# Optimization experiments

Measured on AMD Instinct MI355X. Metric: run time of the kernel, lower is better.

## Reference

```python
import jax, jax.numpy as jnp
import numpy as np

INPUT_DIM = 100
LATENT_DIM = 128
HIDDEN_DIM = 64
BATCH = 16384


def setup_inputs() -> dict:
    key = jax.random.key(0)
    ku, k1, kb1, k2, kb2 = jax.random.split(key, 5)
    u = jax.random.normal(ku, (BATCH, INPUT_DIM), dtype=jnp.float32)
    # PyTorch Linear init: U(-1/sqrt(fan_in), 1/sqrt(fan_in))
    s1 = 1.0 / np.sqrt(INPUT_DIM)
    s2 = 1.0 / np.sqrt(HIDDEN_DIM)
    W1 = jax.random.uniform(k1, (LATENT_DIM, HIDDEN_DIM, INPUT_DIM), jnp.float32, -s1, s1)
    b1 = jax.random.uniform(kb1, (LATENT_DIM, HIDDEN_DIM), jnp.float32, -s1, s1)
    W2 = jax.random.uniform(k2, (LATENT_DIM, HIDDEN_DIM), jnp.float32, -s2, s2)  # out_features=1 squeezed
    b2 = jax.random.uniform(kb2, (LATENT_DIM,), jnp.float32, -s2, s2)
    return {"u": u, "W1": W1, "b1": b1, "W2": W2, "b2": b2}


def reference(u, W1, b1, W2, b2):
    # All latent_dim branches batched as one grouped GEMM.
    # h: [batch, latent, hidden]
    h = jnp.tanh(jnp.einsum('bi,khi->bkh', u, W1) + b1[None, :, :])
    # out: [batch, latent]  (second Linear has output dim 1, squeezed)
    out = jnp.einsum('bkh,kh->bk', h, W2) + b2[None, :]
    return out
```

## Files before the change

kernel.cpp:

```cpp
#include <hip/hip_runtime.h>

#define BATCH 16384
#define LATENT 128
#define HIDDEN 64
#define INDIM 100
#define KPAD 128
#define TANH_SCALE 2.885390081777927f

typedef short shortx8 __attribute__((ext_vector_type(8)));
typedef float floatx4 __attribute__((ext_vector_type(4)));

__device__ __forceinline__ short f2bf(float f) {
    union { float f; unsigned u; } v; v.f = f;
    unsigned r = v.u + 0x7FFF + ((v.u >> 16) & 1);
    return (short)(r >> 16);
}

#if __has_builtin(__builtin_amdgcn_exp2f)
#define EXP2F(x) __builtin_amdgcn_exp2f(x)
#else
#define EXP2F(x) __exp2f(x)
#endif
#if __has_builtin(__builtin_amdgcn_rcpf)
#define RCPF(x) __builtin_amdgcn_rcpf(x)
#else
#define RCPF(x) (1.0f / (x))
#endif

#define N_U_CHUNKS (BATCH * KPAD / 8)
#define N_W_CHUNKS (LATENT * HIDDEN * KPAD / 8)

__global__ __launch_bounds__(256) void prep_all(const float* __restrict__ u,
                                                const float* __restrict__ W1,
                                                const float* __restrict__ b1,
                                                const float* __restrict__ W2,
                                                const float* __restrict__ b2,
                                                shortx8* __restrict__ uf,
                                                shortx8* __restrict__ wf,
                                                float* __restrict__ b2eff) {
    int c = blockIdx.x * 256 + threadIdx.x;
    if (c < N_U_CHUNKS) {
        int lane = c & 63;
        int kt = (c >> 6) & 3;
        int g = c >> 8;
        int row = g * 16 + (lane & 15);
        int kbase = kt * 32 + ((lane >> 4) << 3);
        shortx8 v;
        if (kbase + 7 < INDIM) {
            const float4* p = (const float4*)(u + row * INDIM + kbase);
            float4 f0 = p[0], f1 = p[1];
            v[0] = f2bf(f0.x); v[1] = f2bf(f0.y); v[2] = f2bf(f0.z); v[3] = f2bf(f0.w);
            v[4] = f2bf(f1.x); v[5] = f2bf(f1.y); v[6] = f2bf(f1.z); v[7] = f2bf(f1.w);
        } else {
#pragma unroll
            for (int j = 0; j < 8; j++) {
                int k = kbase + j;
                float f = (k < INDIM) ? u[row * INDIM + k] : (k == INDIM ? 1.0f : 0.0f);
                v[j] = f2bf(f);
            }
        }
        uf[c] = v;
    } else if (c < N_U_CHUNKS + N_W_CHUNKS) {
        int c2 = c - N_U_CHUNKS;
        int lane = c2 & 63;
        int kt = (c2 >> 6) & 3;
        int nt = (c2 >> 8) & 3;
        int lat = c2 >> 10;
        int h = nt * 16 + (lane & 15);
        int hw = lat * HIDDEN + h;
        int kbase = kt * 32 + ((lane >> 4) << 3);
        shortx8 v;
        if (kbase + 7 < INDIM) {
            const float4* p = (const float4*)(W1 + hw * INDIM + kbase);
            float4 f0 = p[0], f1 = p[1];
            v[0] = f2bf(f0.x * TANH_SCALE); v[1] = f2bf(f0.y * TANH_SCALE);
            v[2] = f2bf(f0.z * TANH_SCALE); v[3] = f2bf(f0.w * TANH_SCALE);
            v[4] = f2bf(f1.x * TANH_SCALE); v[5] = f2bf(f1.y * TANH_SCALE);
            v[6] = f2bf(f1.z * TANH_SCALE); v[7] = f2bf(f1.w * TANH_SCALE);
        } else {
#pragma unroll
            for (int j = 0; j < 8; j++) {
                int k = kbase + j;
                float f = (k < INDIM) ? W1[hw * INDIM + k] * TANH_SCALE
                                      : (k == INDIM ? b1[hw] * TANH_SCALE : 0.0f);
                v[j] = f2bf(f);
            }
        }
        wf[c2] = v;
    } else {
        int lat = c - (N_U_CHUNKS + N_W_CHUNKS);
        if (lat < LATENT) {
            float s = b2[lat];
            const float* wp = W2 + lat * HIDDEN;
#pragma unroll 8
            for (int h = 0; h < HIDDEN; h++) s += wp[h];
            b2eff[lat] = s;
        }
    }
}

__global__ __launch_bounds__(256, 4) void branch_mlp(const shortx8* __restrict__ uf,
                                                     const shortx8* __restrict__ wf,
                                                     const float* __restrict__ W2,
                                                     const float* __restrict__ b2eff,
                                                     float* __restrict__ out) {
    int tid = threadIdx.x;
    int lane = tid & 63;
    int w = tid >> 6;
    int bx = blockIdx.x;
    int lat = bx >> 5;
    int G0 = (bx & 31) * 32 + w * 8;
    int q = lane >> 4;

    shortx8 afr[4][4];
    const shortx8* wb = wf + (size_t)lat * 16 * 64 + lane;
#pragma unroll
    for (int nt = 0; nt < 4; nt++)
#pragma unroll
        for (int kt = 0; kt < 4; kt++)
            afr[nt][kt] = wb[(nt * 4 + kt) * 64];

    float4 w2v[4];
#pragma unroll
    for (int nt = 0; nt < 4; nt++) {
        float4 t = *(const float4*)(W2 + lat * HIDDEN + nt * 16 + q * 4);
        w2v[nt] = make_float4(-2.0f * t.x, -2.0f * t.y, -2.0f * t.z, -2.0f * t.w);
    }
    float b2v = b2eff[lat];

    const shortx8* ua = uf + (size_t)G0 * 4 * 64 + lane;
    float* outp = out + (size_t)G0 * 16 * LATENT + lat;

#pragma unroll
    for (int g = 0; g < 8; g++) {
        shortx8 ub[4];
#pragma unroll
        for (int kt = 0; kt < 4; kt++)
            ub[kt] = ua[(g * 4 + kt) * 64];

        floatx4 acc[4] = {};
#pragma unroll
        for (int kt = 0; kt < 4; kt++)
#pragma unroll
            for (int nt = 0; nt < 4; nt++)
                acc[nt] = __builtin_amdgcn_mfma_f32_16x16x32_bf16(afr[nt][kt], ub[kt], acc[nt], 0, 0, 0);

        float s = 0.0f;
#pragma unroll
        for (int nt = 0; nt < 4; nt++)
#pragma unroll
            for (int r = 0; r < 4; r++) {
                float e = EXP2F(acc[nt][r]);
                float rr = RCPF(e + 1.0f);
                s = fmaf((&w2v[nt].x)[r], rr, s);
            }
        s += __shfl_xor(s, 16, 64);
        s += __shfl_xor(s, 32, 64);
        if (lane < 16)
            outp[(g * 16 + lane) * LATENT] = s + b2v;
    }
}

__global__ __launch_bounds__(256) void fallback_kernel(const float* __restrict__ u, const float* __restrict__ W1,
                                                       const float* __restrict__ b1, const float* __restrict__ W2,
                                                       const float* __restrict__ b2, float* __restrict__ out) {
    int idx = blockIdx.x * 256 + threadIdx.x;
    if (idx >= BATCH * LATENT) return;
    int b = idx >> 7;
    int lat = idx & 127;
    const float* ub = u + b * INDIM;
    float s = 0.0f;
    for (int h = 0; h < HIDDEN; h++) {
        const float* wp = W1 + (lat * HIDDEN + h) * INDIM;
        float dd = b1[lat * HIDDEN + h];
        for (int k = 0; k < INDIM; k++) dd += ub[k] * wp[k];
        s += tanhf(dd) * W2[lat * HIDDEN + h];
    }
    out[idx] = s + b2[lat];
}

extern "C" void kernel_launch(void* const* d_in, const int* in_sizes, int n_in,
                              void* d_out, int out_size, void* d_ws, size_t ws_size,
                              hipStream_t stream) {
    const float* u  = (const float*)d_in[0];
    const float* W1 = (const float*)d_in[1];
    const float* b1 = (const float*)d_in[2];
    const float* W2 = (const float*)d_in[3];
    const float* b2 = (const float*)d_in[4];
    float* out = (float*)d_out;

    const size_t UF_BYTES = (size_t)BATCH * KPAD * 2;
    const size_t WF_BYTES = (size_t)LATENT * HIDDEN * KPAD * 2;
    const size_t B2_BYTES = LATENT * sizeof(float);

    if (ws_size < UF_BYTES + WF_BYTES + B2_BYTES) {
        fallback_kernel<<<(BATCH * LATENT + 255) / 256, 256, 0, stream>>>(u, W1, b1, W2, b2, out);
        return;
    }

    shortx8* uf = (shortx8*)d_ws;
    shortx8* wf = (shortx8*)((char*)d_ws + UF_BYTES);
    float* b2eff = (float*)((char*)d_ws + UF_BYTES + WF_BYTES);

    prep_all<<<(N_U_CHUNKS + N_W_CHUNKS) / 256 + 1, 256, 0, stream>>>(u, W1, b1, W2, b2, uf, wf, b2eff);
    branch_mlp<<<4096, 256, 0, stream>>>(uf, wf, W2, b2eff, out);
}
```

Measured before the change: 112.8 us.

## Stage prep conversion through LDS for coalesced loads and batch output shuffles

The prep kernel now processes 16-row tiles per block. It reads the fp32 rows with coalesced float2 loads, converts them to bf16 into a padded LDS tile, then writes the MFMA fragment layout from LDS. The old version had each thread gather strided float4 pairs from scattered rows. In the main kernel, the cross-lane reductions and output stores for all 8 groups are deferred until after the compute loop, so the shuffles are batched and the loop can overlap better. The cost is one LDS buffer and a barrier in prep, plus 8 extra live registers in the main kernel.

```diff
diff --git a/kernel.cpp b/kernel.cpp
--- a/kernel.cpp
+++ b/kernel.cpp
@@ -10,10 +10,9 @@
 typedef short shortx8 __attribute__((ext_vector_type(8)));
 typedef float floatx4 __attribute__((ext_vector_type(4)));
 
-__device__ __forceinline__ short f2bf(float f) {
+__device__ __forceinline__ unsigned bfbits(float f) {
     union { float f; unsigned u; } v; v.f = f;
-    unsigned r = v.u + 0x7FFF + ((v.u >> 16) & 1);
-    return (short)(r >> 16);
+    return (v.u + 0x7FFF + ((v.u >> 16) & 1)) >> 16;
 }
 
 #if __has_builtin(__builtin_amdgcn_exp2f)
@@ -27,8 +26,8 @@
 #define RCPF(x) (1.0f / (x))
 #endif
 
-#define N_U_CHUNKS (BATCH * KPAD / 8)
-#define N_W_CHUNKS (LATENT * HIDDEN * KPAD / 8)
+#define N_U_BLK (BATCH / 16)
+#define N_W_BLK (LATENT * HIDDEN / 16)
 
 __global__ __launch_bounds__(256) void prep_all(const float* __restrict__ u,
                                                 const float* __restrict__ W1,
@@ -38,64 +37,52 @@
                                                 shortx8* __restrict__ uf,
                                                 shortx8* __restrict__ wf,
                                                 float* __restrict__ b2eff) {
-    int c = blockIdx.x * 256 + threadIdx.x;
-    if (c < N_U_CHUNKS) {
-        int lane = c & 63;
-        int kt = (c >> 6) & 3;
-        int g = c >> 8;
-        int row = g * 16 + (lane & 15);
-        int kbase = kt * 32 + ((lane >> 4) << 3);
-        shortx8 v;
-        if (kbase + 7 < INDIM) {
-            const float4* p = (const float4*)(u + row * INDIM + kbase);
-            float4 f0 = p[0], f1 = p[1];
-            v[0] = f2bf(f0.x); v[1] = f2bf(f0.y); v[2] = f2bf(f0.z); v[3] = f2bf(f0.w);
-            v[4] = f2bf(f1.x); v[5] = f2bf(f1.y); v[6] = f2bf(f1.z); v[7] = f2bf(f1.w);
-        } else {
-#pragma unroll
-            for (int j = 0; j < 8; j++) {
-                int k = kbase + j;
-                float f = (k < INDIM) ? u[row * INDIM + k] : (k == INDIM ? 1.0f : 0.0f);
-                v[j] = f2bf(f);
-            }
-        }
-        uf[c] = v;
-    } else if (c < N_U_CHUNKS + N_W_CHUNKS) {
-        int c2 = c - N_U_CHUNKS;
-        int lane = c2 & 63;
-        int kt = (c2 >> 6) & 3;
-        int nt = (c2 >> 8) & 3;
-        int lat = c2 >> 10;
-        int h = nt * 16 + (lane & 15);
-        int hw = lat * HIDDEN + h;
-        int kbase = kt * 32 + ((lane >> 4) << 3);
-        shortx8 v;
-        if (kbase + 7 < INDIM) {
-            const float4* p = (const float4*)(W1 + hw * INDIM + kbase);
-            float4 f0 = p[0], f1 = p[1];
-            v[0] = f2bf(f0.x * TANH_SCALE); v[1] = f2bf(f0.y * TANH_SCALE);
-            v[2] = f2bf(f0.z * TANH_SCALE); v[3] = f2bf(f0.w * TANH_SCALE);
-            v[4] = f2bf(f1.x * TANH_SCALE); v[5] = f2bf(f1.y * TANH_SCALE);
-            v[6] = f2bf(f1.z * TANH_SCALE); v[7] = f2bf(f1.w * TANH_SCALE);
-        } else {
-#pragma unroll
-            for (int j = 0; j < 8; j++) {
-                int k = kbase + j;
-                float f = (k < INDIM) ? W1[hw * INDIM + k] * TANH_SCALE
-                                      : (k == INDIM ? b1[hw] * TANH_SCALE : 0.0f);
-                v[j] = f2bf(f);
-            }
-        }
-        wf[c2] = v;
-    } else {
-        int lat = c - (N_U_CHUNKS + N_W_CHUNKS);
-        if (lat < LATENT) {
-            float s = b2[lat];
-            const float* wp = W2 + lat * HIDDEN;
+    int bx = blockIdx.x;
+    int tid = threadIdx.x;
+
+    if (bx >= N_U_BLK + N_W_BLK) {
+        if (tid < LATENT) {
+            float s = b2[tid];
+            const float* wp = W2 + tid * HIDDEN;
 #pragma unroll 8
             for (int h = 0; h < HIDDEN; h++) s += wp[h];
-            b2eff[lat] = s;
+            b2eff[tid] = s;
         }
+        return;
+    }
+
+    bool isW = (bx >= N_U_BLK);
+    int tileIdx = isW ? (bx - N_U_BLK) : bx;
+    int r0 = tileIdx * 16;
+    const float* src = isW ? W1 : u;
+    float scale = isW ? TANH_SCALE : 1.0f;
+
+    __shared__ short lds[16 * 136];
+
+#pragma unroll
+    for (int it = 0; it < 4; it++) {
+        int p = it * 256 + tid;
+        int rl = p >> 6;
+        int kp = (p & 63) * 2;
+        float f0 = 0.0f, f1 = 0.0f;
+        if (kp < INDIM) {
+            const float2 t = *(const float2*)(src + (r0 + rl) * INDIM + kp);
+            f0 = t.x * scale; f1 = t.y * scale;
+        } else if (kp == INDIM) {
+            f0 = isW ? b1[r0 + rl] * TANH_SCALE : 1.0f;
+        }
+        *(unsigned*)(&lds[rl * 136 + kp]) = bfbits(f0) | (bfbits(f1) << 16);
+    }
+    __syncthreads();
+
+    {
+        int lane = tid & 63;
+        int kt = tid >> 6;
+        int rl = lane & 15;
+        int kb = kt * 32 + ((lane >> 4) << 3);
+        shortx8 v = *(const shortx8*)(&lds[rl * 136 + kb]);
+        shortx8* dst = isW ? wf : uf;
+        dst[((size_t)tileIdx * 4 + kt) * 64 + lane] = v;
     }
 }
 
@@ -129,8 +116,8 @@
     float b2v = b2eff[lat];
 
     const shortx8* ua = uf + (size_t)G0 * 4 * 64 + lane;
-    float* outp = out + (size_t)G0 * 16 * LATENT + lat;
-
+
+    float sg[8];
 #pragma unroll
     for (int g = 0; g < 8; g++) {
         shortx8 ub[4];
@@ -154,10 +141,18 @@
                 float rr = RCPF(e + 1.0f);
                 s = fmaf((&w2v[nt].x)[r], rr, s);
             }
-        s += __shfl_xor(s, 16, 64);
-        s += __shfl_xor(s, 32, 64);
-        if (lane < 16)
-            outp[(g * 16 + lane) * LATENT] = s + b2v;
+        sg[g] = s;
+    }
+
+#pragma unroll
+    for (int g = 0; g < 8; g++) sg[g] += __shfl_xor(sg[g], 16, 64);
+#pragma unroll
+    for (int g = 0; g < 8; g++) sg[g] += __shfl_xor(sg[g], 32, 64);
+    if (lane < 16) {
+        float* outp = out + ((size_t)G0 * 16 + lane) * LATENT + lat;
+#pragma unroll
+        for (int g = 0; g < 8; g++)
+            outp[g * 16 * LATENT] = sg[g] + b2v;
     }
 }
 
@@ -202,6 +197,6 @@
     shortx8* wf = (shortx8*)((char*)d_ws + UF_BYTES);
     float* b2eff = (float*)((char*)d_ws + UF_BYTES + WF_BYTES);
 
-    prep_all<<<(N_U_CHUNKS + N_W_CHUNKS) / 256 + 1, 256, 0, stream>>>(u, W1, b1, W2, b2, uf, wf, b2eff);
+    prep_all<<<N_U_BLK + N_W_BLK + 1, 256, 0, stream>>>(u, W1, b1, W2, b2, uf, wf, b2eff);
     branch_mlp<<<4096, 256, 0, stream>>>(uf, wf, W2, b2eff, out);
 }
```

Measured after the change: 114.0 us. Within noise of the previous version (+1.0%).
